# Kernel optimization log

Measured on AMD Instinct MI355X. Metric: run time of the kernel, lower is better.

## Reference

```python
import math
import jax, jax.numpy as jnp
from jax import lax
import numpy as np

PATCHES = [(8, 8), (4, 4), (2, 2), (1, 1)]  # (width, height) per scale
BN_EPS = 1e-5


def setup_inputs() -> dict:
    key = jax.random.key(0)
    ks = jax.random.split(key, 9)
    b, d, h, w = 4, 256, 64, 64
    s = 1.0 / math.sqrt(d)
    return {
        "x": jax.random.normal(ks[0], (b, d, h, w), jnp.float32),
        "wq": jax.random.normal(ks[1], (d, d), jnp.float32) * s,
        "bq": jax.random.normal(ks[2], (d,), jnp.float32) * 0.02,
        "wk": jax.random.normal(ks[3], (d, d), jnp.float32) * s,
        "bk": jax.random.normal(ks[4], (d,), jnp.float32) * 0.02,
        "wv": jax.random.normal(ks[5], (d, d), jnp.float32) * s,
        "bv": jax.random.normal(ks[6], (d,), jnp.float32) * 0.02,
        "w_out": jax.random.normal(ks[7], (d, d, 3, 3), jnp.float32) * (s / 3.0),
        "b_out": jax.random.normal(ks[8], (d,), jnp.float32) * 0.02,
        "gamma": jnp.ones((d,), jnp.float32),
        "beta": jnp.zeros((d,), jnp.float32),
    }


def _to_tokens(t, b, dk, out_h, ph, out_w, pw):
    # [b, dk, h, w] -> [b, out_h*out_w, dk*ph*pw]
    t = t.reshape(b, dk, out_h, ph, out_w, pw)
    t = t.transpose(0, 2, 4, 1, 3, 5)
    return t.reshape(b, out_h * out_w, dk * ph * pw)


def reference(x, wq, bq, wk, bk, wv, bv, w_out, b_out, gamma, beta):
    b, c, h, w = x.shape
    # 1x1 conv projections == channel matmuls
    q = jnp.einsum('bchw,oc->bohw', x, wq) + bq[None, :, None, None]
    k = jnp.einsum('bchw,oc->bohw', x, wk) + bk[None, :, None, None]
    v = jnp.einsum('bchw,oc->bohw', x, wv) + bv[None, :, None, None]

    dk = c // len(PATCHES)
    outs = []
    for i, (pw, ph) in enumerate(PATCHES):
        sl = slice(i * dk, (i + 1) * dk)
        out_h, out_w = h // ph, w // pw
        Q = _to_tokens(q[:, sl], b, dk, out_h, ph, out_w, pw)
        K = _to_tokens(k[:, sl], b, dk, out_h, ph, out_w, pw)
        V = _to_tokens(v[:, sl], b, dk, out_h, ph, out_w, pw)
        scores = jnp.einsum('bnd,bmd->bnm', Q, K) / math.sqrt(Q.shape[-1])
        p = jax.nn.softmax(scores, axis=-1)
        y = jnp.einsum('bnm,bmd->bnd', p, V)
        # tokens -> [b, dk, h, w]
        y = y.reshape(b, out_h, out_w, dk, ph, pw)
        y = y.transpose(0, 3, 1, 4, 2, 5).reshape(b, dk, h, w)
        outs.append(y)
    out = jnp.concatenate(outs, axis=1)

    # 3x3 conv, padding=1
    z = lax.conv_general_dilated(out, w_out, (1, 1), 'SAME',
                                 dimension_numbers=('NCHW', 'OIHW', 'NCHW'))
    z = z + b_out[None, :, None, None]
    # BatchNorm2d (training-mode batch stats)
    mean = jnp.mean(z, axis=(0, 2, 3), keepdims=True)
    var = jnp.var(z, axis=(0, 2, 3), keepdims=True)
    zn = (z - mean) * lax.rsqrt(var + BN_EPS)
    zn = zn * gamma[None, :, None, None] + beta[None, :, None, None]
    # LeakyReLU(0.2)
    return jnp.where(zn > 0, zn, 0.2 * zn)
```

## Files before the change

### kernel.cpp

```cpp
#include <hip/hip_runtime.h>
#include <cmath>


#define OFF_XB  0LL
#define OFF_QB  2097152LL
#define OFF_SS  8388608LL
#define OFF_PP  12582912LL
#define OFF_YT  14680064LL
#define OFF_WQK 18874368LL
#define OFF_BIA 18972672LL
#define OFF_WCV 18973440LL
#define OFF_STT 19268352LL
#define OFF_SP0 19268864LL
#define OFF_S1  19399936LL
#define OFF_P0  19662080LL
#define OFF_P1  19670272LL
#define OFF_LI  19801344LL

#define FC 0.18033688f
#define CSHIFT 6.0f

typedef __attribute__((ext_vector_type(8))) short short8;
typedef __attribute__((ext_vector_type(4))) float f32x4;

__device__ inline unsigned short f2bf(float f) {
  unsigned u = __float_as_uint(f);
  u += 0x7fff + ((u >> 16) & 1);
  return (unsigned short)(u >> 16);
}

__device__ inline unsigned cvt_pk_bf16(float a, float b) {
  unsigned r;
  asm("v_cvt_pk_bf16_f32 %0, %1, %2" : "=v"(r) : "v"(a), "v"(b));
  return r;
}

__global__ __launch_bounds__(256) void prep_k(
    const float* __restrict__ x, unsigned short* __restrict__ xb,
    const float* __restrict__ wq, const float* __restrict__ wk,
    const float* __restrict__ wv, const float* __restrict__ bq,
    const float* __restrict__ bk, const float* __restrict__ bv,
    unsigned short* __restrict__ Wqkv, float* __restrict__ biasQKV,
    const float* __restrict__ wcv, unsigned short* __restrict__ Wcb)
{
  const int bid = blockIdx.x, t = threadIdx.x;
  if (bid < 256) {
    __shared__ unsigned short rowb[256][66];
    const int b = bid >> 6, y = bid & 63;
    for (int i = t; i < 16384; i += 256) {
      int c = i >> 6, xx = i & 63;
      rowb[c][xx] = f2bf(x[((long long)(b*256 + c) << 12) + (y << 6) + xx]);
    }
    __syncthreads();
    unsigned int* outw = (unsigned int*)(xb + ((long long)bid << 14));
    for (int i = t; i < 8192; i += 256) {
      int xx = i >> 7, c2 = (i & 127) * 2;
      outw[xx*128 + (c2 >> 1)] = (unsigned)rowb[c2][xx]
                               | ((unsigned)rowb[c2+1][xx] << 16);
    }
  } else if (bid < 1024) {
    const int row = bid - 256;
    const int which = row >> 8, oc = row & 255;
    const float* src = which == 0 ? wq : which == 1 ? wk : wv;
    Wqkv[row*256 + t] = f2bf(src[oc*256 + t]);
    if (row < 3) {
      const float* bs = row == 0 ? bq : row == 1 ? bk : bv;
      biasQKV[row*256 + t] = bs[t];
    }
  } else {
    int i = (bid - 1024)*256 + t;
    int tap = i >> 16, oc = (i >> 8) & 255, ic = i & 255;
    Wcb[i] = f2bf(wcv[((long long)(oc*256 + ic))*9 + tap]);
  }
}

template<int EPI, int SH = 0>
__device__ void gemm_nt_body(
    const unsigned short* __restrict__ A, const unsigned short* __restrict__ B,
    void* __restrict__ Cv, const float* __restrict__ bias,
    int M, int N, int K, int lda, int ldb, int ldc,
    long long sA, long long sB, long long sC, float alpha,
    int bx, int by, int bz)
{
  const int t = threadIdx.x, l = t & 63;
  const int lr = l & 15, lg = l >> 4;
  const int w = t >> 6, wm = w >> 1, wn = w & 1;
  const int m0 = by*128 + wm*64, n0 = bx*128 + wn*64;
  if (m0 >= M || n0 >= N) return;
  const unsigned short* Ab = A + (long long)bz*sA + (long long)(m0 + lr)*lda + lg*8;
  const unsigned short* Bb = B + (long long)bz*sB + (long long)(n0 + lr)*ldb + lg*8;

  f32x4 acc[4][4] = {};
#pragma unroll 2
  for (int kk = 0; kk < K; kk += 32) {
    short8 af[4], bf[4];
#pragma unroll
    for (int i = 0; i < 4; i++)
      af[i] = *(const short8*)(Ab + (long long)i*16*lda + kk);
#pragma unroll
    for (int i = 0; i < 4; i++)
      bf[i] = *(const short8*)(Bb + (long long)i*16*ldb + kk);
#pragma unroll
    for (int mf = 0; mf < 4; mf++)
#pragma unroll
      for (int nf = 0; nf < 4; nf++)
        acc[mf][nf] = __builtin_amdgcn_mfma_f32_16x16x32_bf16(
            af[mf], bf[nf], acc[mf][nf], 0, 0, 0);
  }

  if (EPI == 0) {
    float* C = (float*)Cv + (long long)bz*sC;
#pragma unroll
    for (int mf = 0; mf < 4; mf++)
#pragma unroll
      for (int r = 0; r < 4; r++) {
        const int row = m0 + mf*16 + lg*4 + r;
#pragma unroll
        for (int nf = 0; nf < 4; nf++)
          C[(long long)row*ldc + n0 + nf*16 + lr] = acc[mf][nf][r] * alpha;
      }
  } else if (EPI == 1) {
    unsigned short* Qbase = (unsigned short*)Cv;
#pragma unroll
    for (int mf = 0; mf < 4; mf++)
#pragma unroll
      for (int r = 0; r < 4; r++) {
        const int gi = m0 + mf*16 + lg*4 + r;
        const int which = gi >> 8, ch = gi & 255;
        const int scale = ch >> 6, c = ch & 63;
        const int sh = 3 - scale, msk = (1 << sh) - 1;
        const bool tr = (which == 2);
        const float bb = bias[gi];
        unsigned short* dst = Qbase + (long long)which*4194304
                            + (long long)scale*1048576 + (long long)bz*262144;
#pragma unroll
        for (int nf = 0; nf < 4; nf++) {
          const int gj = n0 + nf*16 + lr;
          const int y = gj >> 6, xx = gj & 63;
          const int n = (y >> sh)*(64 >> sh) + (xx >> sh);
          const int d = (c << (2*sh)) + ((y & msk) << sh) + (xx & msk);
          const long long idx = tr
              ? (long long)d*(4096 >> (2*sh)) + n
              : (long long)n*(64 << (2*sh)) + d;
          dst[idx] = f2bf(acc[mf][nf][r] + bb);
        }
      }
  } else {
    unsigned short* inb = (unsigned short*)Cv;
    constexpr int msk = (1 << SH) - 1;
    constexpr int scale = 3 - SH;
#pragma unroll
    for (int mf = 0; mf < 4; mf++)
#pragma unroll
      for (int r = 0; r < 4; r++) {
        const int gi = m0 + mf*16 + lg*4 + r;
        const int ty = gi >> (6 - SH), tx = gi & ((64 >> SH) - 1);
#pragma unroll
        for (int nf = 0; nf < 4; nf++) {
          const int gj = n0 + nf*16 + lr;
          const int c = gj >> (2*SH);
          const int y = (ty << SH) | ((gj >> SH) & msk);
          const int x = (tx << SH) | (gj & msk);
          inb[((((long long)bz << 12) + (y << 6) + x) << 8) + scale*64 + c]
              = f2bf(acc[mf][nf][r]);
        }
      }
  }
}

__global__ __launch_bounds__(256) void qkv_k(
    const unsigned short* __restrict__ Wqkv, const unsigned short* __restrict__ xb,
    unsigned short* __restrict__ Qu, const float* __restrict__ biasQKV)
{
  gemm_nt_body<1>(Wqkv, xb, (void*)Qu, biasQKV, 768, 4096, 256, 256, 256, 0,
                  0, 1048576, 0, 1.0f, blockIdx.x, blockIdx.y, blockIdx.z);
}

__device__ void s0_scores_wave(
    const unsigned short* __restrict__ Q, const unsigned short* __restrict__ K,
    float* __restrict__ Sp, int bid)
{
  const int t = threadIdx.x, l = t & 63, w = t >> 6;
  const int lr = l & 15, lg = l >> 4;
  const int task = bid*4 + w;
  const int b = task >> 3, ks = task & 7;
  const unsigned short* Qb = Q + (long long)b*262144;
  const unsigned short* Kb = K + (long long)b*262144;
  f32x4 acc[4][4] = {};
  const int k0 = ks*512;
#pragma unroll 2
  for (int kk = k0; kk < k0 + 512; kk += 32) {
    short8 af[4], bf[4];
#pragma unroll
    for (int i = 0; i < 4; i++)
      af[i] = *(const short8*)(Qb + (long long)(i*16 + lr)*4096 + kk + lg*8);
#pragma unroll
    for (int i = 0; i < 4; i++)
      bf[i] = *(const short8*)(Kb + (long long)(i*16 + lr)*4096 + kk + lg*8);
#pragma unroll
    for (int mf = 0; mf < 4; mf++)
#pragma unroll
      for (int nf = 0; nf < 4; nf++)
        acc[mf][nf] = __builtin_amdgcn_mfma_f32_16x16x32_bf16(
            af[mf], bf[nf], acc[mf][nf], 0, 0, 0);
  }
#pragma unroll
  for (int mf = 0; mf < 4; mf++)
#pragma unroll
    for (int r = 0; r < 4; r++) {
      const int row = mf*16 + lg*4 + r;
#pragma unroll
      for (int nf = 0; nf < 4; nf++)
        Sp[(((long long)(ks*4 + b)*64 + row) << 6) + nf*16 + lr]
            = acc[mf][nf][r];
    }
}

__device__ void flash3_body(
    const unsigned short* __restrict__ Q3, const unsigned short* __restrict__ K3,
    const unsigned short* __restrict__ Vt3, float* __restrict__ part,
    float* __restrict__ lig, int bx, int b, int sp)
{
  constexpr int LD = 72;
  __shared__ unsigned short Ks[64*LD];
  __shared__ unsigned short Vs[64*LD];
  __shared__ unsigned short Ps[64*LD];
  const int t = threadIdx.x, l = t & 63, w = t >> 6;
  const int lr = l & 15, lg = l >> 4;
  const int q0 = bx * 64;
  const long long base = (long long)b * 262144;
  const unsigned short* Qg = Q3 + base;
  const unsigned short* Kg = K3 + base;
  const unsigned short* Vg = Vt3 + base;

  short8 bq[2];
  bq[0] = *(const short8*)(Qg + (long long)(q0 + w*16 + lr)*64 + lg*8);
  bq[1] = *(const short8*)(Qg + (long long)(q0 + w*16 + lr)*64 + 32 + lg*8);

  f32x4 acc[4] = {};
  float li = 0.f;

  const int r_ = t >> 3, c8_ = (t & 7) * 8;
  for (int kt = sp*16; kt < sp*16 + 16; kt++) {
    const int k0 = kt * 64;
    __syncthreads();
#pragma unroll
    for (int it = 0; it < 2; it++) {
      const int rr = r_ + it*32;
      *(uint4*)(Ks + rr*LD + c8_) =
          *(const uint4*)(Kg + (long long)(k0 + rr)*64 + c8_);
      *(uint4*)(Vs + rr*LD + c8_) =
          *(const uint4*)(Vg + (long long)rr*4096 + k0 + c8_);
    }
    __syncthreads();
    f32x4 s[4];
#pragma unroll
    for (int cf = 0; cf < 4; cf++) {
      short8 ak0 = *(const short8*)(Ks + (cf*16 + lr)*LD + lg*8);
      short8 ak1 = *(const short8*)(Ks + (cf*16 + lr)*LD + 32 + lg*8);
      f32x4 zz = {};
      zz = __builtin_amdgcn_mfma_f32_16x16x32_bf16(ak0, bq[0], zz, 0,0,0);
      s[cf] = __builtin_amdgcn_mfma_f32_16x16x32_bf16(ak1, bq[1], zz, 0,0,0);
    }
    float p[16], psum = 0.f;
#pragma unroll
    for (int cf = 0; cf < 4; cf++)
#pragma unroll
      for (int r = 0; r < 4; r++) {
        float e = exp2f(fmaf(s[cf][r], FC, -CSHIFT));
        p[cf*4 + r] = e; psum += e;
      }
    li += psum;
    {
      unsigned short* pr = Ps + (w*16 + lr)*LD;
#pragma unroll
      for (int cf = 0; cf < 4; cf++) {
        *(unsigned*)(pr + cf*16 + lg*4)     = cvt_pk_bf16(p[cf*4+0], p[cf*4+1]);
        *(unsigned*)(pr + cf*16 + lg*4 + 2) = cvt_pk_bf16(p[cf*4+2], p[cf*4+3]);
      }
    }
    short8 bp0 = *(const short8*)(Ps + (w*16 + lr)*LD + lg*8);
    short8 bp1 = *(const short8*)(Ps + (w*16 + lr)*LD + 32 + lg*8);
#pragma unroll
    for (int df = 0; df < 4; df++) {
      short8 av0 = *(const short8*)(Vs + (df*16 + lr)*LD + lg*8);
      short8 av1 = *(const short8*)(Vs + (df*16 + lr)*LD + 32 + lg*8);
      acc[df] = __builtin_amdgcn_mfma_f32_16x16x32_bf16(av0, bp0, acc[df], 0,0,0);
      acc[df] = __builtin_amdgcn_mfma_f32_16x16x32_bf16(av1, bp1, acc[df], 0,0,0);
    }
  }
  li += __shfl_xor(li, 16);
  li += __shfl_xor(li, 32);
  const long long prow = (long long)(sp*4 + b)*4096 + q0 + w*16 + lr;
#pragma unroll
  for (int df = 0; df < 4; df++)
    *(float4*)(part + prow*64 + df*16 + lg*4) =
        make_float4(acc[df][0], acc[df][1], acc[df][2], acc[df][3]);
  if (lg == 0) lig[prow] = li;
}

__global__ __launch_bounds__(256) void stageA_k(
    const unsigned short* __restrict__ Qu, const unsigned short* __restrict__ Ku,
    const unsigned short* __restrict__ Vu,
    float* __restrict__ Sp0, float* __restrict__ S1, float* __restrict__ S2,
    float* __restrict__ part, float* __restrict__ lig)
{
  const int bid = blockIdx.x;
  if (bid < 1024) {
    flash3_body(Qu+3145728, Ku+3145728, Vu+3145728, part, lig,
                bid & 63, (bid >> 6) & 3, bid >> 8);
  } else if (bid < 1032) {
    s0_scores_wave(Qu, Ku, Sp0, bid - 1024);
  } else if (bid < 1048) {
    int q = bid - 1032;
    gemm_nt_body<0>(Qu+1048576, Ku+1048576, (void*)S1, nullptr,
        256, 256, 1024, 1024, 1024, 256, 262144, 262144, 65536, 0.03125f,
        q & 1, (q >> 1) & 1, q >> 2);
  } else {
    int q = bid - 1048;
    gemm_nt_body<0>(Qu+2097152, Ku+2097152, (void*)S2, nullptr,
        1024, 1024, 256, 256, 256, 1024, 262144, 262144, 1048576, 0.0625f,
        q & 7, (q >> 3) & 7, q >> 6);
  }
}

template<int CNT>
__device__ void softmax_row(const float* __restrict__ S,
                            unsigned short* __restrict__ P, long long row)
{
  const int l = threadIdx.x & 63;
  const float* p = S + row*(CNT*64);
  unsigned short* o = P + row*(CNT*64);
  float v[CNT];
  float mx = -1e30f;
#pragma unroll
  for (int i = 0; i < CNT; i++) { v[i] = p[i*64 + l]; mx = fmaxf(mx, v[i]); }
#pragma unroll
  for (int off = 1; off < 64; off <<= 1) mx = fmaxf(mx, __shfl_xor(mx, off, 64));
  float sum = 0.f;
#pragma unroll
  for (int i = 0; i < CNT; i++) { v[i] = __expf(v[i] - mx); sum += v[i]; }
#pragma unroll
  for (int off = 1; off < 64; off <<= 1) sum += __shfl_xor(sum, off, 64);
  const float inv = 1.f / sum;
#pragma unroll
  for (int i = 0; i < CNT; i++) o[i*64 + l] = f2bf(v[i] * inv);
}

__global__ __launch_bounds__(256) void stageB_k(
    const float* __restrict__ Sp0, unsigned short* __restrict__ P0,
    const float* __restrict__ S1, unsigned short* __restrict__ P1,
    const float* __restrict__ S2, unsigned short* __restrict__ P2,
    const float* __restrict__ part, const float* __restrict__ lig,
    unsigned short* __restrict__ inb)
{
  const int bid = blockIdx.x, t = threadIdx.x, l = t & 63, w = t >> 6;
  if (bid < 1024) {
    softmax_row<16>(S2, P2, (long long)bid*4 + w);
  } else if (bid < 1280) {
    softmax_row<4>(S1, P1, (long long)(bid - 1024)*4 + w);
  } else if (bid < 1344) {
    const int row = (bid - 1280)*4 + w;
    const int b = row >> 6, r = row & 63;
    float v = 0.f;
#pragma unroll
    for (int ks = 0; ks < 8; ks++)
      v += Sp0[(((long long)(ks*4 + b)*64 + r) << 6) + l];
    v *= 0.015625f;
    float mx = v;
#pragma unroll
    for (int off = 1; off < 64; off <<= 1) mx = fmaxf(mx, __shfl_xor(mx, off, 64));
    float e = __expf(v - mx), sum = e;
#pragma unroll
    for (int off = 1; off < 64; off <<= 1) sum += __shfl_xor(sum, off, 64);
    P0[(row << 6) + l] = f2bf(e / sum);
  } else {
    const long long row = (long long)(bid - 1344)*64 + (t >> 2);
    const int dd = (t & 3) * 16;
    float L = 0.f;
#pragma unroll
    for (int s = 0; s < 4; s++) L += lig[(long long)s*16384 + row];
    const float inv = 1.f / L;
#pragma unroll
    for (int j = 0; j < 4; j++) {
      float ax = 0.f, ay = 0.f, az = 0.f, aw = 0.f;
#pragma unroll
      for (int s = 0; s < 4; s++) {
        float4 v = *(const float4*)(part + ((long long)s*16384 + row)*64 + dd + j*4);
        ax += v.x; ay += v.y; az += v.z; aw += v.w;
      }
      ushort4 ov;
      ov.x = f2bf(ax*inv); ov.y = f2bf(ay*inv);
      ov.z = f2bf(az*inv); ov.w = f2bf(aw*inv);
      *(ushort4*)(inb + row*256 + 192 + dd + j*4) = ov;
    }
  }
}

__global__ __launch_bounds__(256) void stageC_k(
    const unsigned short* __restrict__ P0, const unsigned short* __restrict__ P1,
    const unsigned short* __restrict__ P2, const unsigned short* __restrict__ Vu,
    unsigned short* __restrict__ inb)
{
  const int bid = blockIdx.x;
  if (bid < 128) {
    int q = bid;
    gemm_nt_body<2,3>(P0, Vu, (void*)inb, nullptr,
        64, 4096, 64, 64, 64, 0, 4096, 262144, 0, 1.0f,
        q & 31, 0, q >> 5);
  } else if (bid < 192) {
    int q = bid - 128;
    gemm_nt_body<2,2>(P1, Vu+1048576, (void*)inb, nullptr,
        256, 1024, 256, 256, 256, 0, 65536, 262144, 0, 1.0f,
        q & 7, (q >> 3) & 1, q >> 4);
  } else {
    int q = bid - 192;
    gemm_nt_body<2,1>(P2, Vu+2097152, (void*)inb, nullptr,
        1024, 256, 1024, 1024, 1024, 0, 1048576, 262144, 0, 1.0f,
        q & 1, (q >> 1) & 7, q >> 4);
  }
}

__global__ __launch_bounds__(256) void conv_mfma_k(
    const unsigned short* __restrict__ inb, const unsigned short* __restrict__ Wb,
    const float* __restrict__ bias, float* __restrict__ z)
{
  __shared__ unsigned short lds[6*66*40];
  const int t = threadIdx.x;
  const int l = t & 63, waveN = t >> 6;
  const int lr = l & 15, lg = l >> 4;
  const int b = blockIdx.x >> 4, y0 = (blockIdx.x & 15) * 4;
  const int oc0 = blockIdx.y * 32;
  const long long inbase = (long long)b * 1048576;
  const int kgrp = lg * 8;

  f32x4 acc[2][4] = {};

  for (int ic0 = 0; ic0 < 256; ic0 += 32) {
    __syncthreads();
    for (int q = t; q < 1584; q += 256) {
      int ic8 = q & 3, cc = (q >> 2) % 66, rr = q / 264;
      int gy = y0 - 1 + rr, gx = cc - 1;
      uint4 v = make_uint4(0u, 0u, 0u, 0u);
      if ((unsigned)gy < 64u && (unsigned)gx < 64u)
        v = *(const uint4*)(inb + inbase + ((long long)(gy*64 + gx))*256
                            + ic0 + ic8*8);
      *(uint4*)(lds + (q >> 2)*40 + ic8*8) = v;
    }
    __syncthreads();
    const unsigned short* wbase = Wb + (long long)(oc0 + lr)*256 + ic0 + kgrp;
#pragma unroll
    for (int ky = 0; ky < 3; ky++) {
#pragma unroll
      for (int kx = 0; kx < 3; kx++) {
        const int tap = ky*3 + kx;
        short8 a0 = *(const short8*)(wbase + (long long)tap*65536);
        short8 a1 = *(const short8*)(wbase + (long long)tap*65536 + 16*256);
#pragma unroll
        for (int nf = 0; nf < 4; nf++) {
          int pix = waveN*64 + nf*16 + lr;
          int rp = pix >> 6, xx = pix & 63;
          short8 bf = *(const short8*)(lds + ((rp + ky)*66 + xx + kx)*40 + kgrp);
          acc[0][nf] = __builtin_amdgcn_mfma_f32_16x16x32_bf16(a0, bf, acc[0][nf], 0, 0, 0);
          acc[1][nf] = __builtin_amdgcn_mfma_f32_16x16x32_bf16(a1, bf, acc[1][nf], 0, 0, 0);
        }
      }
    }
  }
  const long long zb = ((long long)b * 256) << 12;
#pragma unroll
  for (int mf = 0; mf < 2; mf++) {
#pragma unroll
    for (int r = 0; r < 4; r++) {
      const int oc = oc0 + mf*16 + lg*4 + r;
      const float bb = bias[oc];
      const long long rowbase = zb + ((long long)oc << 12) + y0*64;
#pragma unroll
      for (int nf = 0; nf < 4; nf++) {
        int pix = waveN*64 + nf*16 + lr;
        z[rowbase + pix] = acc[mf][nf][r] + bb;
      }
    }
  }
}

__global__ __launch_bounds__(256) void bn_stats_k(
    const float* __restrict__ z, float* __restrict__ stats)
{
  const int ch = blockIdx.x, t = threadIdx.x;
  float s = 0.f, q = 0.f;
  for (int b = 0; b < 4; b++) {
    const float* p = z + ((long long)(b*256 + ch) << 12);
    for (int i = t; i < 4096; i += 256) { float v = p[i]; s += v; q += v*v; }
  }
  __shared__ float rs[256], rq[256];
  rs[t] = s; rq[t] = q; __syncthreads();
  for (int st = 128; st > 0; st >>= 1) {
    if (t < st) { rs[t] += rs[t+st]; rq[t] += rq[t+st]; }
    __syncthreads();
  }
  if (t == 0) {
    float mean = rs[0] * (1.f/16384.f);
    float var  = rq[0] * (1.f/16384.f) - mean*mean;
    stats[ch]       = mean;
    stats[256 + ch] = rsqrtf(var + 1e-5f);
  }
}

__global__ __launch_bounds__(256) void bn_apply_k(
    const float* __restrict__ z, const float* __restrict__ stats,
    const float* __restrict__ gamma, const float* __restrict__ beta,
    float* __restrict__ out)
{
  long long i4 = ((long long)blockIdx.x*256 + threadIdx.x) * 4;
  int ch = (int)((i4 >> 12) & 255);
  float mean = stats[ch], rsg = stats[256 + ch];
  float g = gamma[ch], bt = beta[ch];
  float4 v = *(const float4*)(z + i4);
  float r[4] = {v.x, v.y, v.z, v.w};
#pragma unroll
  for (int j = 0; j < 4; j++) {
    float u = (r[j] - mean) * rsg * g + bt;
    r[j] = u > 0.f ? u : 0.2f * u;
  }
  *(float4*)(out + i4) = make_float4(r[0], r[1], r[2], r[3]);
}

extern "C" void kernel_launch(void* const* d_in, const int* in_sizes, int n_in,
                              void* d_out, int out_size, void* d_ws, size_t ws_size,
                              hipStream_t stream)
{
  const float* x     = (const float*)d_in[0];
  const float* wq    = (const float*)d_in[1];
  const float* bq    = (const float*)d_in[2];
  const float* wk    = (const float*)d_in[3];
  const float* bk    = (const float*)d_in[4];
  const float* wv    = (const float*)d_in[5];
  const float* bv    = (const float*)d_in[6];
  const float* w_out = (const float*)d_in[7];
  const float* b_out = (const float*)d_in[8];
  const float* gamma = (const float*)d_in[9];
  const float* beta  = (const float*)d_in[10];
  float* out = (float*)d_out;

  float* ws = (float*)d_ws;
  unsigned short* xb  = (unsigned short*)(ws + OFF_XB);
  unsigned short* Qu  = (unsigned short*)(ws + OFF_QB);
  unsigned short* Ku  = Qu + 4194304;
  unsigned short* Vu  = Qu + 8388608;
  float* S2  = ws + OFF_SS;
  unsigned short* P2 = (unsigned short*)(ws + OFF_PP);
  float* part = ws + OFF_YT;
  unsigned short* Wqk = (unsigned short*)(ws + OFF_WQK);
  float* biasQ = ws + OFF_BIA;
  unsigned short* Wcv = (unsigned short*)(ws + OFF_WCV);
  float* St  = ws + OFF_STT;
  float* Sp0 = ws + OFF_SP0;
  float* S1  = ws + OFF_S1;
  unsigned short* P0 = (unsigned short*)(ws + OFF_P0);
  unsigned short* P1 = (unsigned short*)(ws + OFF_P1);
  float* lig = ws + OFF_LI;
  unsigned short* inb = (unsigned short*)(ws + OFF_XB);
  float* z = ws + OFF_YT;

  dim3 blk(256);

  prep_k<<<dim3(3328), blk, 0, stream>>>(
      x, xb, wq, wk, wv, bq, bk, bv, Wqk, biasQ, w_out, Wcv);

  qkv_k<<<dim3(32,6,4), blk, 0, stream>>>(Wqk, xb, Qu, biasQ);

  stageA_k<<<dim3(1304), blk, 0, stream>>>(Qu, Ku, Vu, Sp0, S1, S2, part, lig);

  stageB_k<<<dim3(1600), blk, 0, stream>>>(
      Sp0, P0, S1, P1, S2, P2, part, lig, inb);

  stageC_k<<<dim3(256), blk, 0, stream>>>(P0, P1, P2, Vu, inb);

  conv_mfma_k<<<dim3(64,8), blk, 0, stream>>>(inb, Wcv, b_out, z);

  bn_stats_k<<<dim3(256), blk, 0, stream>>>(z, St);
  bn_apply_k<<<dim3(4096), blk, 0, stream>>>(z, St, gamma, beta, out);
}
```

Before: 261.5 us.

## Fuse flash split-K reduction into attention kernel via in-block LDS combine

The scale-3 flash attention now gives each block 16 queries and splits the 4096 keys across its 4 waves. The waves' partial outputs and row sums are combined in shared memory, and the normalized bf16 result is written straight into the conv input buffer. This drops the fp32 partial/row-sum buffers and the merge branch in the softmax kernel, which also launches fewer blocks. K and V tiles are now read directly from global memory per wave instead of being staged in LDS. Each block therefore reads the whole K/V of its batch, which raises L2 traffic.

```diff
diff --git a/kernel.cpp b/kernel.cpp
--- a/kernel.cpp
+++ b/kernel.cpp
@@ -15,7 +15,6 @@
 #define OFF_S1  19399936LL
 #define OFF_P0  19662080LL
 #define OFF_P1  19670272LL
-#define OFF_LI  19801344LL
 
 #define FC 0.18033688f
 #define CSHIFT 6.0f
@@ -218,46 +217,36 @@
 
 __device__ void flash3_body(
     const unsigned short* __restrict__ Q3, const unsigned short* __restrict__ K3,
-    const unsigned short* __restrict__ Vt3, float* __restrict__ part,
-    float* __restrict__ lig, int bx, int b, int sp)
+    const unsigned short* __restrict__ Vt3, unsigned short* __restrict__ inb,
+    int qg, int b)
 {
   constexpr int LD = 72;
-  __shared__ unsigned short Ks[64*LD];
-  __shared__ unsigned short Vs[64*LD];
   __shared__ unsigned short Ps[64*LD];
+  __shared__ float accL[3*1088];
+  __shared__ float liL[48];
   const int t = threadIdx.x, l = t & 63, w = t >> 6;
   const int lr = l & 15, lg = l >> 4;
-  const int q0 = bx * 64;
+  const int q0 = qg * 16;
   const long long base = (long long)b * 262144;
   const unsigned short* Qg = Q3 + base;
   const unsigned short* Kg = K3 + base;
   const unsigned short* Vg = Vt3 + base;
 
   short8 bq[2];
-  bq[0] = *(const short8*)(Qg + (long long)(q0 + w*16 + lr)*64 + lg*8);
-  bq[1] = *(const short8*)(Qg + (long long)(q0 + w*16 + lr)*64 + 32 + lg*8);
+  bq[0] = *(const short8*)(Qg + (long long)(q0 + lr)*64 + lg*8);
+  bq[1] = *(const short8*)(Qg + (long long)(q0 + lr)*64 + 32 + lg*8);
 
   f32x4 acc[4] = {};
   float li = 0.f;
 
-  const int r_ = t >> 3, c8_ = (t & 7) * 8;
-  for (int kt = sp*16; kt < sp*16 + 16; kt++) {
-    const int k0 = kt * 64;
-    __syncthreads();
-#pragma unroll
-    for (int it = 0; it < 2; it++) {
-      const int rr = r_ + it*32;
-      *(uint4*)(Ks + rr*LD + c8_) =
-          *(const uint4*)(Kg + (long long)(k0 + rr)*64 + c8_);
-      *(uint4*)(Vs + rr*LD + c8_) =
-          *(const uint4*)(Vg + (long long)rr*4096 + k0 + c8_);
-    }
-    __syncthreads();
+  for (int i = 0; i < 16; i++) {
+    const int k0 = (w*16 + i) * 64;
     f32x4 s[4];
 #pragma unroll
     for (int cf = 0; cf < 4; cf++) {
-      short8 ak0 = *(const short8*)(Ks + (cf*16 + lr)*LD + lg*8);
-      short8 ak1 = *(const short8*)(Ks + (cf*16 + lr)*LD + 32 + lg*8);
+      const unsigned short* kr = Kg + (long long)(k0 + cf*16 + lr)*64 + lg*8;
+      short8 ak0 = *(const short8*)(kr);
+      short8 ak1 = *(const short8*)(kr + 32);
       f32x4 zz = {};
       zz = __builtin_amdgcn_mfma_f32_16x16x32_bf16(ak0, bq[0], zz, 0,0,0);
       s[cf] = __builtin_amdgcn_mfma_f32_16x16x32_bf16(ak1, bq[1], zz, 0,0,0);
@@ -283,32 +272,53 @@
     short8 bp1 = *(const short8*)(Ps + (w*16 + lr)*LD + 32 + lg*8);
 #pragma unroll
     for (int df = 0; df < 4; df++) {
-      short8 av0 = *(const short8*)(Vs + (df*16 + lr)*LD + lg*8);
-      short8 av1 = *(const short8*)(Vs + (df*16 + lr)*LD + 32 + lg*8);
+      const unsigned short* vr = Vg + (long long)(df*16 + lr)*4096 + k0 + lg*8;
+      short8 av0 = *(const short8*)(vr);
+      short8 av1 = *(const short8*)(vr + 32);
       acc[df] = __builtin_amdgcn_mfma_f32_16x16x32_bf16(av0, bp0, acc[df], 0,0,0);
       acc[df] = __builtin_amdgcn_mfma_f32_16x16x32_bf16(av1, bp1, acc[df], 0,0,0);
     }
   }
   li += __shfl_xor(li, 16);
   li += __shfl_xor(li, 32);
-  const long long prow = (long long)(sp*4 + b)*4096 + q0 + w*16 + lr;
-#pragma unroll
-  for (int df = 0; df < 4; df++)
-    *(float4*)(part + prow*64 + df*16 + lg*4) =
-        make_float4(acc[df][0], acc[df][1], acc[df][2], acc[df][3]);
-  if (lg == 0) lig[prow] = li;
+  if (w > 0) {
+#pragma unroll
+    for (int df = 0; df < 4; df++)
+      *(float4*)(accL + (w-1)*1088 + lr*68 + df*16 + lg*4) =
+          make_float4(acc[df][0], acc[df][1], acc[df][2], acc[df][3]);
+    if (l < 16) liL[(w-1)*16 + lr] = li;
+  }
+  __syncthreads();
+  if (w == 0) {
+    const float Lt = li + liL[lr] + liL[16 + lr] + liL[32 + lr];
+    const float inv = 1.f / Lt;
+    const long long row = (long long)b*4096 + q0 + lr;
+    unsigned short* ob = inb + row*256 + 192 + lg*4;
+#pragma unroll
+    for (int df = 0; df < 4; df++) {
+      const int off = lr*68 + df*16 + lg*4;
+      float4 aa = *(float4*)(accL + off);
+      float4 ab = *(float4*)(accL + 1088 + off);
+      float4 ac = *(float4*)(accL + 2176 + off);
+      float r0 = (acc[df][0] + aa.x + ab.x + ac.x) * inv;
+      float r1 = (acc[df][1] + aa.y + ab.y + ac.y) * inv;
+      float r2 = (acc[df][2] + aa.z + ab.z + ac.z) * inv;
+      float r3 = (acc[df][3] + aa.w + ab.w + ac.w) * inv;
+      *(unsigned*)(ob + df*16)     = cvt_pk_bf16(r0, r1);
+      *(unsigned*)(ob + df*16 + 2) = cvt_pk_bf16(r2, r3);
+    }
+  }
 }
 
 __global__ __launch_bounds__(256) void stageA_k(
     const unsigned short* __restrict__ Qu, const unsigned short* __restrict__ Ku,
     const unsigned short* __restrict__ Vu,
     float* __restrict__ Sp0, float* __restrict__ S1, float* __restrict__ S2,
-    float* __restrict__ part, float* __restrict__ lig)
+    unsigned short* __restrict__ inb)
 {
   const int bid = blockIdx.x;
   if (bid < 1024) {
-    flash3_body(Qu+3145728, Ku+3145728, Vu+3145728, part, lig,
-                bid & 63, (bid >> 6) & 3, bid >> 8);
+    flash3_body(Qu+3145728, Ku+3145728, Vu+3145728, inb, bid & 255, bid >> 8);
   } else if (bid < 1032) {
     s0_scores_wave(Qu, Ku, Sp0, bid - 1024);
   } else if (bid < 1048) {
@@ -350,16 +360,14 @@
 __global__ __launch_bounds__(256) void stageB_k(
     const float* __restrict__ Sp0, unsigned short* __restrict__ P0,
     const float* __restrict__ S1, unsigned short* __restrict__ P1,
-    const float* __restrict__ S2, unsigned short* __restrict__ P2,
-    const float* __restrict__ part, const float* __restrict__ lig,
-    unsigned short* __restrict__ inb)
+    const float* __restrict__ S2, unsigned short* __restrict__ P2)
 {
   const int bid = blockIdx.x, t = threadIdx.x, l = t & 63, w = t >> 6;
   if (bid < 1024) {
     softmax_row<16>(S2, P2, (long long)bid*4 + w);
   } else if (bid < 1280) {
     softmax_row<4>(S1, P1, (long long)(bid - 1024)*4 + w);
-  } else if (bid < 1344) {
+  } else {
     const int row = (bid - 1280)*4 + w;
     const int b = row >> 6, r = row & 63;
     float v = 0.f;
@@ -374,26 +382,6 @@
 #pragma unroll
     for (int off = 1; off < 64; off <<= 1) sum += __shfl_xor(sum, off, 64);
     P0[(row << 6) + l] = f2bf(e / sum);
-  } else {
-    const long long row = (long long)(bid - 1344)*64 + (t >> 2);
-    const int dd = (t & 3) * 16;
-    float L = 0.f;
-#pragma unroll
-    for (int s = 0; s < 4; s++) L += lig[(long long)s*16384 + row];
-    const float inv = 1.f / L;
-#pragma unroll
-    for (int j = 0; j < 4; j++) {
-      float ax = 0.f, ay = 0.f, az = 0.f, aw = 0.f;
-#pragma unroll
-      for (int s = 0; s < 4; s++) {
-        float4 v = *(const float4*)(part + ((long long)s*16384 + row)*64 + dd + j*4);
-        ax += v.x; ay += v.y; az += v.z; aw += v.w;
-      }
-      ushort4 ov;
-      ov.x = f2bf(ax*inv); ov.y = f2bf(ay*inv);
-      ov.z = f2bf(az*inv); ov.w = f2bf(aw*inv);
-      *(ushort4*)(inb + row*256 + 192 + dd + j*4) = ov;
-    }
   }
 }
 
@@ -550,7 +538,6 @@
   unsigned short* Vu  = Qu + 8388608;
   float* S2  = ws + OFF_SS;
   unsigned short* P2 = (unsigned short*)(ws + OFF_PP);
-  float* part = ws + OFF_YT;
   unsigned short* Wqk = (unsigned short*)(ws + OFF_WQK);
   float* biasQ = ws + OFF_BIA;
   unsigned short* Wcv = (unsigned short*)(ws + OFF_WCV);
@@ -559,7 +546,6 @@
   float* S1  = ws + OFF_S1;
   unsigned short* P0 = (unsigned short*)(ws + OFF_P0);
   unsigned short* P1 = (unsigned short*)(ws + OFF_P1);
-  float* lig = ws + OFF_LI;
   unsigned short* inb = (unsigned short*)(ws + OFF_XB);
   float* z = ws + OFF_YT;
 
@@ -570,10 +556,9 @@
 
   qkv_k<<<dim3(32,6,4), blk, 0, stream>>>(Wqk, xb, Qu, biasQ);
 
-  stageA_k<<<dim3(1304), blk, 0, stream>>>(Qu, Ku, Vu, Sp0, S1, S2, part, lig);
-
-  stageB_k<<<dim3(1600), blk, 0, stream>>>(
-      Sp0, P0, S1, P1, S2, P2, part, lig, inb);
+  stageA_k<<<dim3(1304), blk, 0, stream>>>(Qu, Ku, Vu, Sp0, S1, S2, inb);
+
+  stageB_k<<<dim3(1344), blk, 0, stream>>>(Sp0, P0, S1, P1, S2, P2);
 
   stageC_k<<<dim3(256), blk, 0, stream>>>(P0, P1, P2, Vu, inb);
 
```

Result: slower. 328.3 us (+25.5%).
